# Kernel optimization log

Hardware: AMD Instinct MI355X
Metric: run time of the kernel (lower is better)

Reference implementation:

```python
import jax, jax.numpy as jnp
import numpy as np

H = 1024
NH = 16
HD = H // NH
EPS = 1e-5


def setup_inputs() -> dict:
    key = jax.random.key(0)
    ks = jax.random.split(key, 16)
    B, LQ, LK = 2, 1024, 2048
    s = 1.0 / np.sqrt(H)
    inp = {
        "query": jax.random.normal(ks[0], (B, LQ, H), jnp.float32),
        "key": jax.random.normal(ks[1], (B, LK, H), jnp.float32),
        "value": jax.random.normal(ks[2], (B, LK, H), jnp.float32),
        "mask": jax.random.randint(ks[3], (B, LQ, LK), 0, 2, jnp.int32),
        "Wq": jax.random.normal(ks[4], (H, H), jnp.float32) * s,
        "bq": jnp.zeros((H,), jnp.float32),
        "Wk": jax.random.normal(ks[5], (H, H), jnp.float32) * s,
        "bk": jnp.zeros((H,), jnp.float32),
        "Wv": jax.random.normal(ks[6], (H, H), jnp.float32) * s,
        "bv": jnp.zeros((H,), jnp.float32),
        "Wo": jax.random.normal(ks[7], (H, H), jnp.float32) * s,
        "bo": jnp.zeros((H,), jnp.float32),
        "ln_g": jnp.ones((H,), jnp.float32),
        "ln_b": jnp.zeros((H,), jnp.float32),
    }
    return inp


def _split_heads(x, B, L):
    # [B, L, H] -> [B, NH, L, HD]
    return x.reshape(B, L, NH, HD).transpose(0, 2, 1, 3)


def reference(query, key, value, mask, Wq, bq, Wk, bk, Wv, bv, Wo, bo, ln_g, ln_b):
    B, LQ, _ = query.shape
    LK = key.shape[1]
    # projections (torch Linear: x @ W.T + b)
    Q = _split_heads(query @ Wq.T + bq, B, LQ)   # [B,NH,LQ,HD]
    K = _split_heads(key   @ Wk.T + bk, B, LK)   # [B,NH,LK,HD]
    V = _split_heads(value @ Wv.T + bv, B, LK)   # [B,NH,LK,HD]
    scores = jnp.einsum('bhqd,bhkd->bhqk', Q, K) / np.sqrt(HD)
    scores = jnp.where(mask[:, None, :, :] == 0, jnp.float32(-1e9), scores)
    attn = jax.nn.softmax(scores, axis=-1)
    # dropout is identity in eval mode
    ctx = jnp.einsum('bhqk,bhkd->bhqd', attn, V)            # [B,NH,LQ,HD]
    ctx = ctx.transpose(0, 2, 1, 3).reshape(B, LQ, H)       # [B,LQ,H]
    out = ctx @ Wo.T + bo
    x = out + query
    mu = jnp.mean(x, axis=-1, keepdims=True)
    var = jnp.mean(jnp.square(x - mu), axis=-1, keepdims=True)
    return (x - mu) / jnp.sqrt(var + EPS) * ln_g + ln_b
```

## Files before the change

### kernel.cpp

```cpp
#include <hip/hip_runtime.h>
#include <hip/hip_bf16.h>

typedef __hip_bfloat16 hbf16;

#define Hdim 1024
#define NHEAD 16
#define HDIM 64
#define BATCH 2
#define LQ 1024
#define LK 2048
#define LN_EPS 1e-5f

typedef __bf16 bfv8 __attribute__((ext_vector_type(8)));
typedef float floatx4 __attribute__((ext_vector_type(4)));
typedef union { bfv8 v; __bf16 b[8]; unsigned short s[8]; } bfu8;

#define BK 32
#define LDS_PITCH 40
#define QT 64
#define KT 64
#define KS_PITCH 72
#define VT_OFF(d) ((d) * 72 + (((d) >> 3) << 3))
#define PS_OFF(r) ((r) * 72 + (((r) >> 2) << 3))

__device__ inline bfv8 cvt2(const float4 x, const float4 y) {
    bfv8 r = {(__bf16)x.x, (__bf16)x.y, (__bf16)x.z, (__bf16)x.w,
              (__bf16)y.x, (__bf16)y.y, (__bf16)y.z, (__bf16)y.w};
    return r;
}

__device__ __forceinline__ void glds16(const void* g, void* l) {
    __builtin_amdgcn_global_load_lds(
        (const __attribute__((address_space(1))) void*)g,
        (__attribute__((address_space(3))) void*)l, 16, 0, 0);
}

__global__ __launch_bounds__(256) void cvt_all(
    const float* __restrict__ q, const float* __restrict__ k,
    const float* __restrict__ v, const float* __restrict__ Wq,
    const float* __restrict__ Wk, const float* __restrict__ Wv,
    const int* __restrict__ mask,
    hbf16* __restrict__ qb, hbf16* __restrict__ kb, hbf16* __restrict__ vb,
    hbf16* __restrict__ Wqb, hbf16* __restrict__ Wkb, hbf16* __restrict__ Wvb,
    unsigned short* __restrict__ mpack) {
    const int blk = blockIdx.x;
    if (blk >= 6656) {
        const int t = blk - 6656;
        const int kt = t & 31;
        const int qb2 = (t >> 5) & 15;
        const int b2 = t >> 9;
        const int tid = threadIdx.x;
        const int w = tid >> 6;
        const int lane = tid & 63;
        const int quad = lane >> 4;
        const int u = lane & 15;
        const int qrow = qb2 * 64 + w * 16 + quad * 4;
        const int kcol = kt * 64 + u;
        const int* mp = mask + (size_t)(b2 * LQ + qrow) * LK + kcol;
        unsigned int bits = 0;
#pragma unroll
        for (int ns = 0; ns < 4; ++ns)
#pragma unroll
            for (int rr = 0; rr < 4; ++rr)
                if (mp[(size_t)rr * LK + ns * 16] != 0)
                    bits |= 1u << (ns * 4 + rr);
        mpack[(size_t)t * 256 + tid] = (unsigned short)bits;
        return;
    }
    const float* src; hbf16* dst; int base;
    if (blk < 1024)      { src = q;  dst = qb;  base = blk; }
    else if (blk < 3072) { src = k;  dst = kb;  base = blk - 1024; }
    else if (blk < 5120) { src = v;  dst = vb;  base = blk - 3072; }
    else if (blk < 5632) { src = Wq; dst = Wqb; base = blk - 5120; }
    else if (blk < 6144) { src = Wk; dst = Wkb; base = blk - 5632; }
    else                 { src = Wv; dst = Wvb; base = blk - 6144; }
    const size_t e = (size_t)base * 2048 + (size_t)threadIdx.x * 8;
    const float4 a = *(const float4*)(src + e);
    const float4 b = *(const float4*)(src + e + 4);
    *(bfv8*)((__bf16*)dst + e) = cvt2(a, b);
}

__global__ __launch_bounds__(256) void proj3_glds(
    const hbf16* __restrict__ qb, const hbf16* __restrict__ kb,
    const hbf16* __restrict__ vb,
    const hbf16* __restrict__ Wqb, const hbf16* __restrict__ Wkb,
    const hbf16* __restrict__ Wvb,
    const float* __restrict__ bq, const float* __restrict__ bk,
    const float* __restrict__ bv,
    hbf16* __restrict__ Qp, hbf16* __restrict__ Kp, hbf16* __restrict__ Vp) {
    const int z = blockIdx.z;
    if (z == 0 && blockIdx.y >= (BATCH * LQ) / 128) return;
    const hbf16* A; const hbf16* W; const float* bias; hbf16* out; float scale;
    if (z == 0)      { A = qb; W = Wqb; bias = bq; out = Qp; scale = 0.125f; }
    else if (z == 1) { A = kb; W = Wkb; bias = bk; out = Kp; scale = 1.0f; }
    else             { A = vb; W = Wvb; bias = bv; out = Vp; scale = 1.0f; }

    __shared__ __align__(16) __bf16 As[2][128 * 32];
    __shared__ __align__(16) __bf16 Bs[2][128 * 32];
    const int tid = threadIdx.x;
    const int lane = tid & 63;
    const int w = tid >> 6;
    const int wm = w & 1, wn = w >> 1;
    const int u = lane & 15;
    const int quad = lane >> 4;
    const int rowBase = blockIdx.y * 128;
    const int colBase = blockIdx.x * 128;

    const int srow = tid >> 2;
    const int scol = (tid & 3) * 8;
    const hbf16* aP = A + (size_t)(rowBase + srow) * Hdim + scol;
    const hbf16* wP = W + (size_t)(colBase + srow) * Hdim + scol;
    const int ldsOff = srow * 32 + scol;

#define P_STAGE(buf, k0)                                            \
    do {                                                            \
        glds16(aP + (k0), &As[buf][ldsOff]);                        \
        glds16(aP + (k0) + (size_t)64 * Hdim, &As[buf][ldsOff + 64 * 32]); \
        glds16(wP + (k0), &Bs[buf][ldsOff]);                        \
        glds16(wP + (k0) + (size_t)64 * Hdim, &Bs[buf][ldsOff + 64 * 32]); \
    } while (0)

    floatx4 acc[4][4];
#pragma unroll
    for (int mi = 0; mi < 4; ++mi)
#pragma unroll
        for (int ni = 0; ni < 4; ++ni) acc[mi][ni] = (floatx4){0.f, 0.f, 0.f, 0.f};

#define P_COMPUTE(buf)                                                         \
    do {                                                                       \
        bfv8 af[4], bf[4];                                                     \
        _Pragma("unroll") for (int mi = 0; mi < 4; ++mi)                       \
            af[mi] = *(const bfv8*)&As[buf][(wm * 64 + mi * 16 + u) * 32 + quad * 8]; \
        _Pragma("unroll") for (int ni = 0; ni < 4; ++ni)                       \
            bf[ni] = *(const bfv8*)&Bs[buf][(wn * 64 + ni * 16 + u) * 32 + quad * 8]; \
        _Pragma("unroll") for (int mi = 0; mi < 4; ++mi)                       \
            _Pragma("unroll") for (int ni = 0; ni < 4; ++ni)                   \
                acc[mi][ni] = __builtin_amdgcn_mfma_f32_16x16x32_bf16(af[mi], bf[ni], acc[mi][ni], 0, 0, 0); \
    } while (0)

    P_STAGE(0, 0);
    __syncthreads();

    for (int t = 0; t < 32; t += 2) {
        if (t + 1 < 32) P_STAGE(1, (t + 1) * 32);
        P_COMPUTE(0);
        __syncthreads();
        if (t + 2 < 32) P_STAGE(0, (t + 2) * 32);
        P_COMPUTE(1);
        __syncthreads();
    }
#undef P_STAGE
#undef P_COMPUTE

#pragma unroll
    for (int mi = 0; mi < 4; ++mi)
#pragma unroll
        for (int ni = 0; ni < 4; ++ni) {
            const int n = colBase + wn * 64 + ni * 16 + u;
            const float bn = bias[n];
#pragma unroll
            for (int rr = 0; rr < 4; ++rr) {
                const int m = rowBase + wm * 64 + mi * 16 + quad * 4 + rr;
                out[(size_t)m * Hdim + n] = __float2bfloat16((acc[mi][ni][rr] + bn) * scale);
            }
        }
}

__global__ __launch_bounds__(256) void gemm_ctx_merge(
    const float* __restrict__ Opart, const float* __restrict__ lpart,
    const float* __restrict__ W, const float* __restrict__ bias,
    const float* __restrict__ resid, float* __restrict__ out) {
    __shared__ __align__(16) __bf16 As[2][64 * 32];
    __shared__ __align__(16) __bf16 Bs[2][64 * 32];
    const int tid = threadIdx.x;
    const int lane = tid & 63;
    const int w = tid >> 6;
    const int wm = w & 1, wn = w >> 1;
    const int u = lane & 15;
    const int quad = lane >> 4;
    const int rowBase = blockIdx.y * 64;
    const int colBase = blockIdx.x * 64;

    const int srow = tid >> 2;
    const int scol = (tid & 3) * 8;
    const size_t mrow = (size_t)(rowBase + srow);
    const float* o0 = Opart + mrow * Hdim + scol;
    const float* o1 = o0 + (size_t)BATCH * LQ * Hdim;
    const float* lp0 = lpart + mrow * NHEAD;
    const float* lp1 = lp0 + BATCH * LQ * NHEAD;
    const float* wP = W + (size_t)(colBase + srow) * Hdim + scol;
    const int ldsOff = srow * 32 + scol;

    floatx4 acc[2][2];
#pragma unroll
    for (int mi = 0; mi < 2; ++mi)
#pragma unroll
        for (int ni = 0; ni < 2; ++ni) acc[mi][ni] = (floatx4){0.f, 0.f, 0.f, 0.f};

#define C_COMPUTE(buf)                                                         \
    do {                                                                       \
        bfv8 af[2], bf[2];                                                     \
        _Pragma("unroll") for (int mi = 0; mi < 2; ++mi)                       \
            af[mi] = *(const bfv8*)&As[buf][(wm * 32 + mi * 16 + u) * 32 + quad * 8]; \
        _Pragma("unroll") for (int ni = 0; ni < 2; ++ni)                       \
            bf[ni] = *(const bfv8*)&Bs[buf][(wn * 32 + ni * 16 + u) * 32 + quad * 8]; \
        _Pragma("unroll") for (int mi = 0; mi < 2; ++mi)                       \
            _Pragma("unroll") for (int ni = 0; ni < 2; ++ni)                   \
                acc[mi][ni] = __builtin_amdgcn_mfma_f32_16x16x32_bf16(af[mi], bf[ni], acc[mi][ni], 0, 0, 0); \
    } while (0)

#define M_WRITEA(buf, a0, a1, c0, c1, l0v, l1v)                                \
    do {                                                                       \
        const float invl_ = 1.0f / ((l0v) + (l1v));                            \
        float4 s0_, s1_;                                                       \
        s0_.x = (a0.x + c0.x) * invl_; s0_.y = (a0.y + c0.y) * invl_;          \
        s0_.z = (a0.z + c0.z) * invl_; s0_.w = (a0.w + c0.w) * invl_;          \
        s1_.x = (a1.x + c1.x) * invl_; s1_.y = (a1.y + c1.y) * invl_;          \
        s1_.z = (a1.z + c1.z) * invl_; s1_.w = (a1.w + c1.w) * invl_;          \
        *(bfv8*)&As[buf][ldsOff] = cvt2(s0_, s1_);                             \
    } while (0)

    {
        const float4 a0 = *(const float4*)(o0);
        const float4 a1 = *(const float4*)(o0 + 4);
        const float4 c0 = *(const float4*)(o1);
        const float4 c1 = *(const float4*)(o1 + 4);
        const int hh = scol >> 6;
        const float l0v = lp0[hh], l1v = lp1[hh];
        const float4* w4 = (const float4*)wP;
        const float4 w0 = w4[0], w1 = w4[1];
        M_WRITEA(0, a0, a1, c0, c1, l0v, l1v);
        *(bfv8*)&Bs[0][ldsOff] = cvt2(w0, w1);
    }
    __syncthreads();

    for (int t = 0; t < 32; t += 2) {
        {
            float4 a0, a1, c0, c1, w0, w1; float l0v = 1.f, l1v = 0.f;
            const bool pf = (t + 1 < 32);
            if (pf) {
                const int kk = (t + 1) * 32;
                a0 = *(const float4*)(o0 + kk);
                a1 = *(const float4*)(o0 + kk + 4);
                c0 = *(const float4*)(o1 + kk);
                c1 = *(const float4*)(o1 + kk + 4);
                const int hh = (kk + scol) >> 6;
                l0v = lp0[hh]; l1v = lp1[hh];
                const float4* w4 = (const float4*)(wP + kk);
                w0 = w4[0]; w1 = w4[1];
            }
            C_COMPUTE(0);
            if (pf) {
                M_WRITEA(1, a0, a1, c0, c1, l0v, l1v);
                *(bfv8*)&Bs[1][ldsOff] = cvt2(w0, w1);
            }
            __syncthreads();
        }
        {
            float4 a0, a1, c0, c1, w0, w1; float l0v = 1.f, l1v = 0.f;
            const bool pf = (t + 2 < 32);
            if (pf) {
                const int kk = (t + 2) * 32;
                a0 = *(const float4*)(o0 + kk);
                a1 = *(const float4*)(o0 + kk + 4);
                c0 = *(const float4*)(o1 + kk);
                c1 = *(const float4*)(o1 + kk + 4);
                const int hh = (kk + scol) >> 6;
                l0v = lp0[hh]; l1v = lp1[hh];
                const float4* w4 = (const float4*)(wP + kk);
                w0 = w4[0]; w1 = w4[1];
            }
            C_COMPUTE(1);
            if (pf) {
                M_WRITEA(0, a0, a1, c0, c1, l0v, l1v);
                *(bfv8*)&Bs[0][ldsOff] = cvt2(w0, w1);
            }
            __syncthreads();
        }
    }
#undef C_COMPUTE
#undef M_WRITEA

#pragma unroll
    for (int mi = 0; mi < 2; ++mi)
#pragma unroll
        for (int ni = 0; ni < 2; ++ni) {
            const int n = colBase + wn * 32 + ni * 16 + u;
            const float bn = bias[n];
#pragma unroll
            for (int rr = 0; rr < 4; ++rr) {
                const int m = rowBase + wm * 32 + mi * 16 + quad * 4 + rr;
                out[(size_t)m * Hdim + n] = acc[mi][ni][rr] + bn + resid[(size_t)m * Hdim + n];
            }
        }
}

__global__ __launch_bounds__(256) void proj3_mfma(
    const float* __restrict__ q_in, const float* __restrict__ k_in,
    const float* __restrict__ v_in,
    const float* __restrict__ Wq, const float* __restrict__ bq,
    const float* __restrict__ Wk, const float* __restrict__ bk,
    const float* __restrict__ Wv, const float* __restrict__ bv,
    hbf16* __restrict__ Qp, hbf16* __restrict__ Kp, hbf16* __restrict__ Vp) {
    const int z = blockIdx.z;
    if (z == 0 && blockIdx.y >= (BATCH * LQ) / 64) return;
    const float* A; const float* W; const float* bias; hbf16* out; float scale;
    if (z == 0)      { A = q_in; W = Wq; bias = bq; out = Qp; scale = 0.125f; }
    else if (z == 1) { A = k_in; W = Wk; bias = bk; out = Kp; scale = 1.0f; }
    else             { A = v_in; W = Wv; bias = bv; out = Vp; scale = 1.0f; }

    __shared__ __align__(16) __bf16 As[64 * LDS_PITCH];
    __shared__ __align__(16) __bf16 Bs[64 * LDS_PITCH];
    const int tid = threadIdx.x;
    const int lane = tid & 63;
    const int w = tid >> 6;
    const int wm = w & 1, wn = w >> 1;
    const int rowBase = blockIdx.y * 64;
    const int colBase = blockIdx.x * 64;
    const int sr = tid >> 2;
    const int scg = (tid & 3) * 8;
    const int lr = lane & 15;
    const int quad = lane >> 4;

    floatx4 acc[2][2] = {};

    for (int k0 = 0; k0 < Hdim; k0 += BK) {
        const float* ap = A + (size_t)(rowBase + sr) * Hdim + k0 + scg;
        bfv8 av = cvt2(((const float4*)ap)[0], ((const float4*)ap)[1]);
        const float* wp = W + (size_t)(colBase + sr) * Hdim + k0 + scg;
        bfv8 bv8 = cvt2(((const float4*)wp)[0], ((const float4*)wp)[1]);
        __syncthreads();
        *(bfv8*)&As[sr * LDS_PITCH + scg] = av;
        *(bfv8*)&Bs[sr * LDS_PITCH + scg] = bv8;
        __syncthreads();

        bfv8 bf[2];
#pragma unroll
        for (int nt = 0; nt < 2; ++nt)
            bf[nt] = *(const bfv8*)&Bs[(wn * 32 + nt * 16 + lr) * LDS_PITCH + quad * 8];
#pragma unroll
        for (int mt = 0; mt < 2; ++mt) {
            bfv8 af = *(const bfv8*)&As[(wm * 32 + mt * 16 + lr) * LDS_PITCH + quad * 8];
#pragma unroll
            for (int nt = 0; nt < 2; ++nt)
                acc[mt][nt] = __builtin_amdgcn_mfma_f32_16x16x32_bf16(af, bf[nt], acc[mt][nt], 0, 0, 0);
        }
    }

#pragma unroll
    for (int mt = 0; mt < 2; ++mt)
#pragma unroll
        for (int nt = 0; nt < 2; ++nt) {
            const int n = colBase + wn * 32 + nt * 16 + lr;
            const float bn = bias[n];
#pragma unroll
            for (int rr = 0; rr < 4; ++rr) {
                const int m = rowBase + wm * 32 + mt * 16 + quad * 4 + rr;
                out[(size_t)m * Hdim + n] = __float2bfloat16((acc[mt][nt][rr] + bn) * scale);
            }
        }
}

__global__ __launch_bounds__(256) void gemm_mfma_f32(const float* __restrict__ A,
                                                     const float* __restrict__ W,
                                                     const float* __restrict__ bias,
                                                     hbf16* __restrict__ out,
                                                     float scale) {
    __shared__ __align__(16) __bf16 As[64 * LDS_PITCH];
    __shared__ __align__(16) __bf16 Bs[64 * LDS_PITCH];
    const int tid = threadIdx.x;
    const int lane = tid & 63;
    const int w = tid >> 6;
    const int wm = w & 1, wn = w >> 1;
    const int rowBase = blockIdx.y * 64;
    const int colBase = blockIdx.x * 64;
    const int sr = tid >> 2;
    const int scg = (tid & 3) * 8;
    const int lr = lane & 15;
    const int quad = lane >> 4;

    floatx4 acc[2][2] = {};

    for (int k0 = 0; k0 < Hdim; k0 += BK) {
        const float* ap = A + (size_t)(rowBase + sr) * Hdim + k0 + scg;
        bfv8 av = cvt2(((const float4*)ap)[0], ((const float4*)ap)[1]);
        const float* wp = W + (size_t)(colBase + sr) * Hdim + k0 + scg;
        bfv8 bv = cvt2(((const float4*)wp)[0], ((const float4*)wp)[1]);
        __syncthreads();
        *(bfv8*)&As[sr * LDS_PITCH + scg] = av;
        *(bfv8*)&Bs[sr * LDS_PITCH + scg] = bv;
        __syncthreads();

        bfv8 bf[2];
#pragma unroll
        for (int nt = 0; nt < 2; ++nt)
            bf[nt] = *(const bfv8*)&Bs[(wn * 32 + nt * 16 + lr) * LDS_PITCH + quad * 8];
#pragma unroll
        for (int mt = 0; mt < 2; ++mt) {
            bfv8 af = *(const bfv8*)&As[(wm * 32 + mt * 16 + lr) * LDS_PITCH + quad * 8];
#pragma unroll
            for (int nt = 0; nt < 2; ++nt)
                acc[mt][nt] = __builtin_amdgcn_mfma_f32_16x16x32_bf16(af, bf[nt], acc[mt][nt], 0, 0, 0);
        }
    }

#pragma unroll
    for (int mt = 0; mt < 2; ++mt)
#pragma unroll
        for (int nt = 0; nt < 2; ++nt) {
            const int n = colBase + wn * 32 + nt * 16 + lr;
            const float bn = bias[n];
#pragma unroll
            for (int rr = 0; rr < 4; ++rr) {
                const int m = rowBase + wm * 32 + mt * 16 + quad * 4 + rr;
                out[(size_t)m * Hdim + n] = __float2bfloat16((acc[mt][nt][rr] + bn) * scale);
            }
        }
}

__global__ __launch_bounds__(256) void gemm_mfma_ctx(const hbf16* __restrict__ A,
                                                     const float* __restrict__ W,
                                                     const float* __restrict__ bias,
                                                     const float* __restrict__ resid,
                                                     float* __restrict__ out) {
    __shared__ __align__(16) __bf16 As[64 * LDS_PITCH];
    __shared__ __align__(16) __bf16 Bs[64 * LDS_PITCH];
    const int tid = threadIdx.x;
    const int lane = tid & 63;
    const int w = tid >> 6;
    const int wm = w & 1, wn = w >> 1;
    const int rowBase = blockIdx.y * 64;
    const int colBase = blockIdx.x * 64;
    const int sr = tid >> 2;
    const int scg = (tid & 3) * 8;
    const int lr = lane & 15;
    const int quad = lane >> 4;

    floatx4 acc[2][2] = {};

    for (int k0 = 0; k0 < Hdim; k0 += BK) {
        bfv8 av = *(const bfv8*)(A + (size_t)(rowBase + sr) * Hdim + k0 + scg);
        const float* wp = W + (size_t)(colBase + sr) * Hdim + k0 + scg;
        bfv8 bv = cvt2(((const float4*)wp)[0], ((const float4*)wp)[1]);
        __syncthreads();
        *(bfv8*)&As[sr * LDS_PITCH + scg] = av;
        *(bfv8*)&Bs[sr * LDS_PITCH + scg] = bv;
        __syncthreads();

        bfv8 bf[2];
#pragma unroll
        for (int nt = 0; nt < 2; ++nt)
            bf[nt] = *(const bfv8*)&Bs[(wn * 32 + nt * 16 + lr) * LDS_PITCH + quad * 8];
#pragma unroll
        for (int mt = 0; mt < 2; ++mt) {
            bfv8 af = *(const bfv8*)&As[(wm * 32 + mt * 16 + lr) * LDS_PITCH + quad * 8];
#pragma unroll
            for (int nt = 0; nt < 2; ++nt)
                acc[mt][nt] = __builtin_amdgcn_mfma_f32_16x16x32_bf16(af, bf[nt], acc[mt][nt], 0, 0, 0);
        }
    }

#pragma unroll
    for (int mt = 0; mt < 2; ++mt)
#pragma unroll
        for (int nt = 0; nt < 2; ++nt) {
            const int n = colBase + wn * 32 + nt * 16 + lr;
            const float bn = bias[n];
#pragma unroll
            for (int rr = 0; rr < 4; ++rr) {
                const int m = rowBase + wm * 32 + mt * 16 + quad * 4 + rr;
                out[(size_t)m * Hdim + n] = acc[mt][nt][rr] + bn + resid[(size_t)m * Hdim + n];
            }
        }
}

__global__ __launch_bounds__(256) void mask_prep_st(const int* __restrict__ mask,
                                                    hbf16* __restrict__ mbias) {
    const int t = blockIdx.x;
    const int kt = t & 31;
    const int qb = (t >> 5) & 15;
    const int b = t >> 9;
    const int tid = threadIdx.x;
    const int w = tid >> 6;
    const int lane = tid & 63;
    const int quad = lane >> 4;
    const int u = lane & 15;
    const int qrow = qb * 64 + w * 16 + quad * 4;
    const int kcol = kt * 64 + u;
    const int* mp = mask + ((size_t)(b * LQ + qrow)) * LK + kcol;

    bfu8 v0, v1;
#pragma unroll
    for (int ns = 0; ns < 4; ++ns)
#pragma unroll
        for (int rr = 0; rr < 4; ++rr) {
            const int mv = mp[(size_t)rr * LK + ns * 16];
            const __bf16 bias = (mv == 0) ? (__bf16)(-1e9f) : (__bf16)(-10.0f);
            const int j = ns * 4 + rr;
            if (j < 8) v0.b[j] = bias; else v1.b[j - 8] = bias;
        }
    __bf16* dst = (__bf16*)mbias + (size_t)t * 4096 + tid * 16;
    *(bfv8*)dst = v0.v;
    *(bfv8*)(dst + 8) = v1.v;
}

__global__ __launch_bounds__(256, 4) void attn_split(const hbf16* __restrict__ Qp,
                                                     const hbf16* __restrict__ Kp,
                                                     const hbf16* __restrict__ Vp,
                                                     const unsigned short* __restrict__ mpack,
                                                     float* __restrict__ Opart,
                                                     float* __restrict__ lpart) {
    const int wg = (blockIdx.x & 7) * 128 + (blockIdx.x >> 3);
    const int qb = wg & 15;
    const int h = (wg >> 4) & 15;
    const int z = wg >> 8;
    const int b = z >> 1;
    const int sp = z & 1;
    const int tid = threadIdx.x;
    const int lane = tid & 63;
    const int w = tid >> 6;
    const int u = lane & 15;
    const int quad = lane >> 4;
    const int qBase = qb * QT;

    __shared__ __align__(16) __bf16 Ks[64 * KS_PITCH];
    __shared__ __align__(16) __bf16 Vt[4672];
    __shared__ __align__(16) __bf16 Ps[4][1184];

    const int qrow_frag = qBase + w * 16 + u;
    const hbf16* qptr = Qp + (size_t)(b * LQ + qrow_frag) * Hdim + h * HDIM + quad * 8;
    const bfv8 af_q0 = *(const bfv8*)qptr;
    const bfv8 af_q1 = *(const bfv8*)(qptr + 32);

    float l_acc[4] = {0.f, 0.f, 0.f, 0.f};
    floatx4 acc_o[4];
#pragma unroll
    for (int nd = 0; nd < 4; ++nd) acc_o[nd] = (floatx4){0.f, 0.f, 0.f, 0.f};

    const int sk = tid >> 2;
    const int sdg = (tid & 3) * 16;
    const int vk2 = (tid >> 3) * 2;
    const int vd0 = (tid & 7) * 8;
    const unsigned short* mpk = mpack + (size_t)((b * 16 + qb) * 32) * 256 + tid;

    const int kt0 = sp * (LK / KT / 2);
    const int ktEnd = kt0 + (LK / KT / 2);

    unsigned int pmw;
    bfu8 pv0, pv1;
    bfv8 pk0, pk1;

#define A_LOADS(kt)                                                            \
    do {                                                                       \
        const int kBase_ = (kt) * KT;                                          \
        pmw = mpk[(size_t)(kt) * 256];                                         \
        const hbf16* vp_ = Vp + (size_t)(b * LK + kBase_ + vk2) * Hdim + h * HDIM + vd0; \
        pv0.v = *(const bfv8*)vp_;                                             \
        pv1.v = *(const bfv8*)(vp_ + Hdim);                                    \
        const hbf16* kp_ = Kp + (size_t)(b * LK + kBase_ + sk) * Hdim + h * HDIM + sdg; \
        pk0 = *(const bfv8*)kp_;                                               \
        pk1 = *(const bfv8*)(kp_ + 8);                                         \
    } while (0)

    A_LOADS(kt0);

    for (int kt = kt0; kt < ktEnd; ++kt) {
        __syncthreads();
        *(bfv8*)&Ks[sk * KS_PITCH + sdg] = pk0;
        *(bfv8*)&Ks[sk * KS_PITCH + sdg + 8] = pk1;
#pragma unroll
        for (int i = 0; i < 8; ++i) {
            unsigned int pk = (unsigned int)pv0.s[i] | ((unsigned int)pv1.s[i] << 16);
            *(unsigned int*)&Vt[VT_OFF(vd0 + i) + vk2] = pk;
        }
        const unsigned int mw = pmw;
        __syncthreads();

        if (kt + 1 < ktEnd) A_LOADS(kt + 1);

        floatx4 acc_s[4];
        __builtin_amdgcn_s_setprio(1);
#pragma unroll
        for (int ns = 0; ns < 4; ++ns) {
            const bfv8 bk0 = *(const bfv8*)&Ks[(ns * 16 + u) * KS_PITCH + quad * 8];
            const bfv8 bk1 = *(const bfv8*)&Ks[(ns * 16 + u) * KS_PITCH + quad * 8 + 32];
            floatx4 a = (floatx4){0.f, 0.f, 0.f, 0.f};
            a = __builtin_amdgcn_mfma_f32_16x16x32_bf16(af_q0, bk0, a, 0, 0, 0);
            a = __builtin_amdgcn_mfma_f32_16x16x32_bf16(af_q1, bk1, a, 0, 0, 0);
            acc_s[ns] = a;
        }
        __builtin_amdgcn_s_setprio(0);

        __bf16* Pw = Ps[w];
#pragma unroll
        for (int ns = 0; ns < 4; ++ns)
#pragma unroll
            for (int rr = 0; rr < 4; ++rr) {
                const int j = ns * 4 + rr;
                const float bias = ((mw >> j) & 1u) ? -10.0f : -1e9f;
                const float p = __expf(acc_s[ns][rr] + bias);
                Pw[PS_OFF(quad * 4 + rr) + ns * 16 + u] = (__bf16)p;
                l_acc[rr] += p;
            }

        const bfv8 af_p0 = *(const bfv8*)&Pw[PS_OFF(u) + quad * 8];
        const bfv8 af_p1 = *(const bfv8*)&Pw[PS_OFF(u) + quad * 8 + 32];
        __builtin_amdgcn_s_setprio(1);
#pragma unroll
        for (int nd = 0; nd < 4; ++nd) {
            const bfv8 bv0 = *(const bfv8*)&Vt[VT_OFF(nd * 16 + u) + quad * 8];
            const bfv8 bv1 = *(const bfv8*)&Vt[VT_OFF(nd * 16 + u) + quad * 8 + 32];
            acc_o[nd] = __builtin_amdgcn_mfma_f32_16x16x32_bf16(af_p0, bv0, acc_o[nd], 0, 0, 0);
            acc_o[nd] = __builtin_amdgcn_mfma_f32_16x16x32_bf16(af_p1, bv1, acc_o[nd], 0, 0, 0);
        }
        __builtin_amdgcn_s_setprio(0);
    }
#undef A_LOADS

#pragma unroll
    for (int rr = 0; rr < 4; ++rr) {
        float l = l_acc[rr];
        l += __shfl_xor(l, 1, 64);
        l += __shfl_xor(l, 2, 64);
        l += __shfl_xor(l, 4, 64);
        l += __shfl_xor(l, 8, 64);
        const int qrow = qBase + w * 16 + quad * 4 + rr;
        const size_t m = (size_t)(b * LQ + qrow);
        float* orow = Opart + (size_t)sp * (BATCH * LQ * Hdim) + m * Hdim + h * HDIM;
#pragma unroll
        for (int nd = 0; nd < 4; ++nd)
            orow[nd * 16 + u] = acc_o[nd][rr];
        if (u == 0)
            lpart[(size_t)sp * (BATCH * LQ * NHEAD) + m * NHEAD + h] = l;
    }
}

__global__ __launch_bounds__(256, 4) void attn_flash_st(const hbf16* __restrict__ Qp,
                                                        const hbf16* __restrict__ Kp,
                                                        const hbf16* __restrict__ Vp,
                                                        const hbf16* __restrict__ mbias,
                                                        hbf16* __restrict__ ctx) {
    const int qb = blockIdx.x;
    const int h = blockIdx.y;
    const int b = blockIdx.z;
    const int tid = threadIdx.x;
    const int lane = tid & 63;
    const int w = tid >> 6;
    const int u = lane & 15;
    const int quad = lane >> 4;
    const int qBase = qb * QT;

    __shared__ __align__(16) __bf16 Ks[64 * KS_PITCH];
    __shared__ __align__(16) __bf16 Vt[4672];
    __shared__ __align__(16) __bf16 Ps[4][1184];

    const int qrow_frag = qBase + w * 16 + u;
    const hbf16* qptr = Qp + (size_t)(b * LQ + qrow_frag) * Hdim + h * HDIM + quad * 8;
    const bfv8 af_q0 = *(const bfv8*)qptr;
    const bfv8 af_q1 = *(const bfv8*)(qptr + 32);

    float l_acc[4] = {0.f, 0.f, 0.f, 0.f};
    floatx4 acc_o[4];
#pragma unroll
    for (int nd = 0; nd < 4; ++nd) acc_o[nd] = (floatx4){0.f, 0.f, 0.f, 0.f};

    const int sk = tid >> 2;
    const int sdg = (tid & 3) * 16;
    const int vk2 = (tid >> 3) * 2;
    const int vd0 = (tid & 7) * 8;
    const __bf16* mbT = (const __bf16*)mbias + (size_t)(b * 16 + qb) * 32 * 4096 + tid * 16;

    for (int kt = 0; kt < LK / KT; ++kt) {
        const int kBase = kt * KT;

        bfu8 mb0, mb1;
        mb0.v = *(const bfv8*)(mbT + (size_t)kt * 4096);
        mb1.v = *(const bfv8*)(mbT + (size_t)kt * 4096 + 8);

        const hbf16* vp0 = Vp + (size_t)(b * LK + kBase + vk2) * Hdim + h * HDIM + vd0;
        bfu8 v0, v1;
        v0.v = *(const bfv8*)vp0;
        v1.v = *(const bfv8*)(vp0 + Hdim);
        const hbf16* kp = Kp + (size_t)(b * LK + kBase + sk) * Hdim + h * HDIM + sdg;
        const bfv8 kv0 = *(const bfv8*)kp;
        const bfv8 kv1 = *(const bfv8*)(kp + 8);

        __syncthreads();
        *(bfv8*)&Ks[sk * KS_PITCH + sdg] = kv0;
        *(bfv8*)&Ks[sk * KS_PITCH + sdg + 8] = kv1;
#pragma unroll
        for (int i = 0; i < 8; ++i) {
            unsigned int pk = (unsigned int)v0.s[i] | ((unsigned int)v1.s[i] << 16);
            *(unsigned int*)&Vt[VT_OFF(vd0 + i) + vk2] = pk;
        }
        __syncthreads();

        floatx4 acc_s[4];
#pragma unroll
        for (int ns = 0; ns < 4; ++ns) {
            const bfv8 bk0 = *(const bfv8*)&Ks[(ns * 16 + u) * KS_PITCH + quad * 8];
            const bfv8 bk1 = *(const bfv8*)&Ks[(ns * 16 + u) * KS_PITCH + quad * 8 + 32];
            floatx4 a = (floatx4){0.f, 0.f, 0.f, 0.f};
            a = __builtin_amdgcn_mfma_f32_16x16x32_bf16(af_q0, bk0, a, 0, 0, 0);
            a = __builtin_amdgcn_mfma_f32_16x16x32_bf16(af_q1, bk1, a, 0, 0, 0);
            acc_s[ns] = a;
        }

        __bf16* Pw = Ps[w];
#pragma unroll
        for (int ns = 0; ns < 4; ++ns)
#pragma unroll
            for (int rr = 0; rr < 4; ++rr) {
                const int j = ns * 4 + rr;
                const float bias = (j < 8) ? (float)mb0.b[j] : (float)mb1.b[j - 8];
                const float p = __expf(acc_s[ns][rr] + bias);
                Pw[PS_OFF(quad * 4 + rr) + ns * 16 + u] = (__bf16)p;
                l_acc[rr] += p;
            }

        const bfv8 af_p0 = *(const bfv8*)&Pw[PS_OFF(u) + quad * 8];
        const bfv8 af_p1 = *(const bfv8*)&Pw[PS_OFF(u) + quad * 8 + 32];
#pragma unroll
        for (int nd = 0; nd < 4; ++nd) {
            const bfv8 bv0 = *(const bfv8*)&Vt[VT_OFF(nd * 16 + u) + quad * 8];
            const bfv8 bv1 = *(const bfv8*)&Vt[VT_OFF(nd * 16 + u) + quad * 8 + 32];
            acc_o[nd] = __builtin_amdgcn_mfma_f32_16x16x32_bf16(af_p0, bv0, acc_o[nd], 0, 0, 0);
            acc_o[nd] = __builtin_amdgcn_mfma_f32_16x16x32_bf16(af_p1, bv1, acc_o[nd], 0, 0, 0);
        }
    }

#pragma unroll
    for (int rr = 0; rr < 4; ++rr) {
        float l = l_acc[rr];
        l += __shfl_xor(l, 1, 64);
        l += __shfl_xor(l, 2, 64);
        l += __shfl_xor(l, 4, 64);
        l += __shfl_xor(l, 8, 64);
        const float invl = 1.0f / l;
        const int qrow = qBase + w * 16 + quad * 4 + rr;
        hbf16* crow = ctx + (size_t)(b * LQ + qrow) * Hdim + h * HDIM;
#pragma unroll
        for (int nd = 0; nd < 4; ++nd)
            crow[nd * 16 + u] = __float2bfloat16(acc_o[nd][rr] * invl);
    }
}

__global__ __launch_bounds__(256) void ln_kernel(float* __restrict__ x,
                                                 const float* __restrict__ g,
                                                 const float* __restrict__ beta) {
    const int row = blockIdx.x;
    float* xr = x + (size_t)row * Hdim;
    __shared__ float red[256];
    const int tid = threadIdx.x;

    const float4 xi = ((const float4*)xr)[tid];
    red[tid] = xi.x + xi.y + xi.z + xi.w;
    __syncthreads();
    for (int st = 128; st > 0; st >>= 1) {
        if (tid < st) red[tid] += red[tid + st];
        __syncthreads();
    }
    const float mu = red[0] * (1.0f / Hdim);
    __syncthreads();
    {
        float dx = xi.x - mu, dy = xi.y - mu, dz = xi.z - mu, dw = xi.w - mu;
        red[tid] = dx * dx + dy * dy + dz * dz + dw * dw;
    }
    __syncthreads();
    for (int st = 128; st > 0; st >>= 1) {
        if (tid < st) red[tid] += red[tid + st];
        __syncthreads();
    }
    const float rstd = rsqrtf(red[0] * (1.0f / Hdim) + LN_EPS);

    const float4 g4 = ((const float4*)g)[tid];
    const float4 b4 = ((const float4*)beta)[tid];
    float4 y;
    y.x = (xi.x - mu) * rstd * g4.x + b4.x;
    y.y = (xi.y - mu) * rstd * g4.y + b4.y;
    y.z = (xi.z - mu) * rstd * g4.z + b4.z;
    y.w = (xi.w - mu) * rstd * g4.w + b4.w;
    ((float4*)xr)[tid] = y;
}

__device__ inline float wave_red_sum(float v) {
    v += __shfl_down(v, 32, 64);
    v += __shfl_down(v, 16, 64);
    v += __shfl_down(v, 8, 64);
    v += __shfl_down(v, 4, 64);
    v += __shfl_down(v, 2, 64);
    v += __shfl_down(v, 1, 64);
    return v;
}

__global__ __launch_bounds__(256) void fused_mha(
    const float* __restrict__ q_in, const float* __restrict__ k_in,
    const float* __restrict__ v_in, const int* __restrict__ mask,
    const float* __restrict__ Wq, const float* __restrict__ bq,
    const float* __restrict__ Wk, const float* __restrict__ bk,
    const float* __restrict__ Wv, const float* __restrict__ bv,
    const float* __restrict__ Wo, const float* __restrict__ bo,
    const float* __restrict__ ln_g, const float* __restrict__ ln_b,
    float* __restrict__ out) {
    const int q = blockIdx.x;
    const int b = blockIdx.y;
    const int tid = threadIdx.x;
    const int lane = tid & 63;
    const int w = tid >> 6;

    __shared__ float qrow[Hdim];
    __shared__ float qt[Hdim];
    __shared__ float sc[LK];
    __shared__ float u[Hdim];
    __shared__ float ctxv[Hdim];
    __shared__ float Qh[HDIM];
    __shared__ float red[256];
    __shared__ float sb_sh;

    const float* qp = q_in + (size_t)(b * LQ + q) * Hdim;
    for (int i = tid; i < Hdim; i += 256) qrow[i] = qp[i];
    __syncthreads();

    const float* keyb = k_in + (size_t)b * LK * Hdim;
    const float* valb = v_in + (size_t)b * LK * Hdim;
    const int* mrow = mask + (size_t)(b * LQ + q) * LK;

    for (int h = 0; h < NHEAD; ++h) {
        for (int dd = w; dd < HDIM; dd += 4) {
            const float4* wrow = (const float4*)(Wq + (size_t)(h * HDIM + dd) * Hdim);
            const float4* q4 = (const float4*)qrow;
            float p = 0.f;
#pragma unroll
            for (int i0 = 0; i0 < 4; ++i0) {
                float4 a = wrow[i0 * 64 + lane];
                float4 c = q4[i0 * 64 + lane];
                p += a.x * c.x + a.y * c.y + a.z * c.z + a.w * c.w;
            }
            p = wave_red_sum(p);
            if (lane == 0) Qh[dd] = p + bq[h * HDIM + dd];
        }
        __syncthreads();

        if (tid < HDIM) red[tid] = Qh[tid] * bk[h * HDIM + tid];

        float4 s4 = {0.f, 0.f, 0.f, 0.f};
        for (int d = 0; d < HDIM; ++d) {
            float4 a = ((const float4*)(Wk + (size_t)(h * HDIM + d) * Hdim))[tid];
            float qd = Qh[d];
            s4.x += a.x * qd;
            s4.y += a.y * qd;
            s4.z += a.z * qd;
            s4.w += a.w * qd;
        }
        __syncthreads();
        if (tid == 0) {
            float s = 0.f;
            for (int i = 0; i < HDIM; ++i) s += red[i];
            sb_sh = s;
        }
        ((float4*)qt)[tid] = s4;
        __syncthreads();
        const float sb = sb_sh;

        for (int k = w; k < LK; k += 4) {
            const float4* krow = (const float4*)(keyb + (size_t)k * Hdim);
            const float4* q4 = (const float4*)qt;
            float p = 0.f;
#pragma unroll
            for (int i0 = 0; i0 < 4; ++i0) {
                float4 a = krow[i0 * 64 + lane];
                float4 c = q4[i0 * 64 + lane];
                p += a.x * c.x + a.y * c.y + a.z * c.z + a.w * c.w;
            }
            p = wave_red_sum(p);
            if (lane == 0) {
                float s = (p + sb) * 0.125f;
                if (mrow[k] == 0) s = -1e9f;
                sc[k] = s;
            }
        }
        __syncthreads();

        float m = -1e30f;
        for (int k = tid; k < LK; k += 256) m = fmaxf(m, sc[k]);
        red[tid] = m;
        __syncthreads();
        for (int s = 128; s > 0; s >>= 1) {
            if (tid < s) red[tid] = fmaxf(red[tid], red[tid + s]);
            __syncthreads();
        }
        const float mx = red[0];
        __syncthreads();
        float sum = 0.f;
        for (int k = tid; k < LK; k += 256) {
            float e = __expf(sc[k] - mx);
            sc[k] = e;
            sum += e;
        }
        red[tid] = sum;
        __syncthreads();
        for (int s = 128; s > 0; s >>= 1) {
            if (tid < s) red[tid] += red[tid + s];
            __syncthreads();
        }
        const float inv = 1.0f / red[0];
        for (int k = tid; k < LK; k += 256) sc[k] *= inv;
        __syncthreads();

        {
            float4 acc = {0.f, 0.f, 0.f, 0.f};
            const float4* vb4 = (const float4*)valb;
#pragma unroll 4
            for (int k = 0; k < LK; ++k) {
                float p = sc[k];
                float4 a = vb4[(size_t)k * (Hdim / 4) + tid];
                acc.x += a.x * p;
                acc.y += a.y * p;
                acc.z += a.z * p;
                acc.w += a.w * p;
            }
            ((float4*)u)[tid] = acc;
        }
        __syncthreads();

        for (int dd = w; dd < HDIM; dd += 4) {
            const float4* wrow = (const float4*)(Wv + (size_t)(h * HDIM + dd) * Hdim);
            const float4* u4 = (const float4*)u;
            float p = 0.f;
#pragma unroll
            for (int i0 = 0; i0 < 4; ++i0) {
                float4 a = wrow[i0 * 64 + lane];
                float4 c = u4[i0 * 64 + lane];
                p += a.x * c.x + a.y * c.y + a.z * c.z + a.w * c.w;
            }
            p = wave_red_sum(p);
            if (lane == 0) ctxv[h * HDIM + dd] = p + bv[h * HDIM + dd];
        }
        __syncthreads();
    }

    for (int n = w; n < Hdim; n += 4) {
        const float4* wrow = (const float4*)(Wo + (size_t)n * Hdim);
        const float4* c4 = (const float4*)ctxv;
        float p = 0.f;
#pragma unroll
        for (int i0 = 0; i0 < 4; ++i0) {
            float4 a = wrow[i0 * 64 + lane];
            float4 c = c4[i0 * 64 + lane];
            p += a.x * c.x + a.y * c.y + a.z * c.z + a.w * c.w;
        }
        p = wave_red_sum(p);
        if (lane == 0) qt[n] = p + bo[n] + qrow[n];
    }
    __syncthreads();

    {
        const float4 x4 = ((const float4*)qt)[tid];
        red[tid] = x4.x + x4.y + x4.z + x4.w;
    }
    __syncthreads();
    for (int s = 128; s > 0; s >>= 1) {
        if (tid < s) red[tid] += red[tid + s];
        __syncthreads();
    }
    const float mu = red[0] * (1.0f / Hdim);
    __syncthreads();
    {
        const float4 x4 = ((const float4*)qt)[tid];
        float dx = x4.x - mu, dy = x4.y - mu, dz = x4.z - mu, dw = x4.w - mu;
        red[tid] = dx * dx + dy * dy + dz * dz + dw * dw;
    }
    __syncthreads();
    for (int s = 128; s > 0; s >>= 1) {
        if (tid < s) red[tid] += red[tid + s];
        __syncthreads();
    }
    const float rstd = rsqrtf(red[0] * (1.0f / Hdim) + LN_EPS);

    float* orow = out + (size_t)(b * LQ + q) * Hdim;
    const float4 x4 = ((const float4*)qt)[tid];
    const float4 g4 = ((const float4*)ln_g)[tid];
    const float4 b4 = ((const float4*)ln_b)[tid];
    float4 y;
    y.x = (x4.x - mu) * rstd * g4.x + b4.x;
    y.y = (x4.y - mu) * rstd * g4.y + b4.y;
    y.z = (x4.z - mu) * rstd * g4.z + b4.z;
    y.w = (x4.w - mu) * rstd * g4.w + b4.w;
    ((float4*)orow)[tid] = y;
}

extern "C" void kernel_launch(void* const* d_in, const int* in_sizes, int n_in,
                              void* d_out, int out_size, void* d_ws, size_t ws_size,
                              hipStream_t stream) {
    const float* query = (const float*)d_in[0];
    const float* key   = (const float*)d_in[1];
    const float* value = (const float*)d_in[2];
    const int*   mask  = (const int*)d_in[3];
    const float* Wq = (const float*)d_in[4];
    const float* bq = (const float*)d_in[5];
    const float* Wk = (const float*)d_in[6];
    const float* bk = (const float*)d_in[7];
    const float* Wv = (const float*)d_in[8];
    const float* bv = (const float*)d_in[9];
    const float* Wo = (const float*)d_in[10];
    const float* bo = (const float*)d_in[11];
    const float* ln_g = (const float*)d_in[12];
    const float* ln_b = (const float*)d_in[13];
    float* out = (float*)d_out;

    const size_t MB = 1024 * 1024;
    dim3 blk(256);

    if (ws_size >= 50 * MB) {
        char* p = (char*)d_ws;
        hbf16* Qp    = (hbf16*)(p + 0 * MB);
        hbf16* Kp    = (hbf16*)(p + 4 * MB);
        hbf16* Vp    = (hbf16*)(p + 12 * MB);
        float* Opart = (float*)(p + 20 * MB);
        unsigned short* mpack = (unsigned short*)(p + 46 * MB);
        float* lpart = (float*)(p + 47 * MB);

        hbf16* qb  = (hbf16*)(p + 20 * MB);
        hbf16* kb  = (hbf16*)(p + 24 * MB);
        hbf16* vb  = (hbf16*)(p + 32 * MB);
        hbf16* Wqb = (hbf16*)(p + 40 * MB);
        hbf16* Wkb = (hbf16*)(p + 42 * MB);
        hbf16* Wvb = (hbf16*)(p + 44 * MB);

        cvt_all<<<dim3(7680), blk, 0, stream>>>(query, key, value, Wq, Wk, Wv,
                                                mask, qb, kb, vb, Wqb, Wkb, Wvb,
                                                mpack);
        proj3_glds<<<dim3(Hdim / 128, (BATCH * LK) / 128, 3), blk, 0, stream>>>(
            qb, kb, vb, Wqb, Wkb, Wvb, bq, bk, bv, Qp, Kp, Vp);

        attn_split<<<dim3(1024), blk, 0, stream>>>(
            Qp, Kp, Vp, mpack, Opart, lpart);

        gemm_ctx_merge<<<dim3(Hdim / 64, (BATCH * LQ) / 64), blk, 0, stream>>>(
            Opart, lpart, Wo, bo, query, out);
        ln_kernel<<<BATCH * LQ, blk, 0, stream>>>(out, ln_g, ln_b);
    } else if (ws_size >= 32 * MB) {
        char* p = (char*)d_ws;
        hbf16* Qp = (hbf16*)p;    p += 4 * MB;
        hbf16* Kp = (hbf16*)p;    p += 8 * MB;
        hbf16* Vp = (hbf16*)p;    p += 8 * MB;
        hbf16* ctxb = (hbf16*)p;  p += 4 * MB;
        hbf16* mbias = (hbf16*)p; p += 8 * MB;

        gemm_mfma_f32<<<dim3(Hdim / 64, (BATCH * LQ) / 64), blk, 0, stream>>>(query, Wq, bq, Qp, 0.125f);
        gemm_mfma_f32<<<dim3(Hdim / 64, (BATCH * LK) / 64), blk, 0, stream>>>(key, Wk, bk, Kp, 1.0f);
        gemm_mfma_f32<<<dim3(Hdim / 64, (BATCH * LK) / 64), blk, 0, stream>>>(value, Wv, bv, Vp, 1.0f);
        mask_prep_st<<<dim3(1024), blk, 0, stream>>>(mask, mbias);
        attn_flash_st<<<dim3(LQ / QT, NHEAD, BATCH), blk, 0, stream>>>(Qp, Kp, Vp, mbias, ctxb);
        gemm_mfma_ctx<<<dim3(Hdim / 64, (BATCH * LQ) / 64), blk, 0, stream>>>(ctxb, Wo, bo, query, out);
        ln_kernel<<<BATCH * LQ, blk, 0, stream>>>(out, ln_g, ln_b);
    } else {
        fused_mha<<<dim3(LQ, BATCH), dim3(256), 0, stream>>>(
            query, key, value, mask, Wq, bq, Wk, bk, Wv, bv, Wo, bo, ln_g, ln_b, out);
    }
}
```

Measured before the change: 240.8 us.

## Fuse fp32-to-bf16 activation conversion into projection GEMM A-tile loads

The separate conversion pass over query/key/value is removed. The projection kernel now loads fp32 activations directly, converts them in registers and writes bf16 into LDS, overlapping this with the MFMA compute on the other buffer. The prep kernel now only converts the weights and packs the mask. The projection grid is also flattened into 640 blocks with a swizzled block-to-tile mapping and no idle Q blocks. This saves a full write and read of the bf16 activation copies, but the A-tile loads go through registers instead of direct global-to-LDS, which adds register pressure and VALU work inside the GEMM loop.

```diff
diff --git a/kernel.cpp b/kernel.cpp
--- a/kernel.cpp
+++ b/kernel.cpp
@@ -35,65 +35,62 @@
         (__attribute__((address_space(3))) void*)l, 16, 0, 0);
 }
 
-__global__ __launch_bounds__(256) void cvt_all(
-    const float* __restrict__ q, const float* __restrict__ k,
-    const float* __restrict__ v, const float* __restrict__ Wq,
-    const float* __restrict__ Wk, const float* __restrict__ Wv,
-    const int* __restrict__ mask,
-    hbf16* __restrict__ qb, hbf16* __restrict__ kb, hbf16* __restrict__ vb,
+__global__ __launch_bounds__(256) void prep_wmask(
+    const float* __restrict__ Wq, const float* __restrict__ Wk,
+    const float* __restrict__ Wv, const int* __restrict__ mask,
     hbf16* __restrict__ Wqb, hbf16* __restrict__ Wkb, hbf16* __restrict__ Wvb,
     unsigned short* __restrict__ mpack) {
     const int blk = blockIdx.x;
-    if (blk >= 6656) {
-        const int t = blk - 6656;
-        const int kt = t & 31;
-        const int qb2 = (t >> 5) & 15;
-        const int b2 = t >> 9;
-        const int tid = threadIdx.x;
-        const int w = tid >> 6;
-        const int lane = tid & 63;
-        const int quad = lane >> 4;
-        const int u = lane & 15;
-        const int qrow = qb2 * 64 + w * 16 + quad * 4;
-        const int kcol = kt * 64 + u;
-        const int* mp = mask + (size_t)(b2 * LQ + qrow) * LK + kcol;
-        unsigned int bits = 0;
-#pragma unroll
-        for (int ns = 0; ns < 4; ++ns)
-#pragma unroll
-            for (int rr = 0; rr < 4; ++rr)
-                if (mp[(size_t)rr * LK + ns * 16] != 0)
-                    bits |= 1u << (ns * 4 + rr);
-        mpack[(size_t)t * 256 + tid] = (unsigned short)bits;
+    if (blk < 1536) {
+        const float* src; hbf16* dst; int base;
+        if (blk < 512)       { src = Wq; dst = Wqb; base = blk; }
+        else if (blk < 1024) { src = Wk; dst = Wkb; base = blk - 512; }
+        else                 { src = Wv; dst = Wvb; base = blk - 1024; }
+        const size_t e = (size_t)base * 2048 + (size_t)threadIdx.x * 8;
+        const float4 a = *(const float4*)(src + e);
+        const float4 b = *(const float4*)(src + e + 4);
+        *(bfv8*)((__bf16*)dst + e) = cvt2(a, b);
         return;
     }
-    const float* src; hbf16* dst; int base;
-    if (blk < 1024)      { src = q;  dst = qb;  base = blk; }
-    else if (blk < 3072) { src = k;  dst = kb;  base = blk - 1024; }
-    else if (blk < 5120) { src = v;  dst = vb;  base = blk - 3072; }
-    else if (blk < 5632) { src = Wq; dst = Wqb; base = blk - 5120; }
-    else if (blk < 6144) { src = Wk; dst = Wkb; base = blk - 5632; }
-    else                 { src = Wv; dst = Wvb; base = blk - 6144; }
-    const size_t e = (size_t)base * 2048 + (size_t)threadIdx.x * 8;
-    const float4 a = *(const float4*)(src + e);
-    const float4 b = *(const float4*)(src + e + 4);
-    *(bfv8*)((__bf16*)dst + e) = cvt2(a, b);
-}
-
-__global__ __launch_bounds__(256) void proj3_glds(
-    const hbf16* __restrict__ qb, const hbf16* __restrict__ kb,
-    const hbf16* __restrict__ vb,
+    const int t = blk - 1536;
+    const int kt = t & 31;
+    const int qb2 = (t >> 5) & 15;
+    const int b2 = t >> 9;
+    const int tid = threadIdx.x;
+    const int w = tid >> 6;
+    const int lane = tid & 63;
+    const int quad = lane >> 4;
+    const int u = lane & 15;
+    const int qrow = qb2 * 64 + w * 16 + quad * 4;
+    const int kcol = kt * 64 + u;
+    const int* mp = mask + (size_t)(b2 * LQ + qrow) * LK + kcol;
+    unsigned int bits = 0;
+#pragma unroll
+    for (int ns = 0; ns < 4; ++ns)
+#pragma unroll
+        for (int rr = 0; rr < 4; ++rr)
+            if (mp[(size_t)rr * LK + ns * 16] != 0)
+                bits |= 1u << (ns * 4 + rr);
+    mpack[(size_t)t * 256 + tid] = (unsigned short)bits;
+}
+
+__global__ __launch_bounds__(256) void proj3_f32(
+    const float* __restrict__ q_in, const float* __restrict__ k_in,
+    const float* __restrict__ v_in,
     const hbf16* __restrict__ Wqb, const hbf16* __restrict__ Wkb,
     const hbf16* __restrict__ Wvb,
     const float* __restrict__ bq, const float* __restrict__ bk,
     const float* __restrict__ bv,
     hbf16* __restrict__ Qp, hbf16* __restrict__ Kp, hbf16* __restrict__ Vp) {
-    const int z = blockIdx.z;
-    if (z == 0 && blockIdx.y >= (BATCH * LQ) / 128) return;
-    const hbf16* A; const hbf16* W; const float* bias; hbf16* out; float scale;
-    if (z == 0)      { A = qb; W = Wqb; bias = bq; out = Qp; scale = 0.125f; }
-    else if (z == 1) { A = kb; W = Wkb; bias = bk; out = Kp; scale = 1.0f; }
-    else             { A = vb; W = Wvb; bias = bv; out = Vp; scale = 1.0f; }
+    const int wg = (blockIdx.x & 7) * 80 + (blockIdx.x >> 3);
+    int z, x, y;
+    if (wg < 128)      { z = 0; x = wg & 7; y = wg >> 3; }
+    else if (wg < 384) { z = 1; x = (wg - 128) & 7; y = (wg - 128) >> 3; }
+    else               { z = 2; x = (wg - 384) & 7; y = (wg - 384) >> 3; }
+    const float* A; const hbf16* W; const float* bias; hbf16* out; float scale;
+    if (z == 0)      { A = q_in; W = Wqb; bias = bq; out = Qp; scale = 0.125f; }
+    else if (z == 1) { A = k_in; W = Wkb; bias = bk; out = Kp; scale = 1.0f; }
+    else             { A = v_in; W = Wvb; bias = bv; out = Vp; scale = 1.0f; }
 
     __shared__ __align__(16) __bf16 As[2][128 * 32];
     __shared__ __align__(16) __bf16 Bs[2][128 * 32];
@@ -103,21 +100,23 @@
     const int wm = w & 1, wn = w >> 1;
     const int u = lane & 15;
     const int quad = lane >> 4;
-    const int rowBase = blockIdx.y * 128;
-    const int colBase = blockIdx.x * 128;
+    const int rowBase = y * 128;
+    const int colBase = x * 128;
+
+    const int arow = tid >> 1;
+    const int acol = (tid & 1) * 16;
+    const float* aPf = A + (size_t)(rowBase + arow) * Hdim + acol;
+    const int ldsOffA = arow * 32 + acol;
 
     const int srow = tid >> 2;
     const int scol = (tid & 3) * 8;
-    const hbf16* aP = A + (size_t)(rowBase + srow) * Hdim + scol;
     const hbf16* wP = W + (size_t)(colBase + srow) * Hdim + scol;
-    const int ldsOff = srow * 32 + scol;
-
-#define P_STAGE(buf, k0)                                            \
-    do {                                                            \
-        glds16(aP + (k0), &As[buf][ldsOff]);                        \
-        glds16(aP + (k0) + (size_t)64 * Hdim, &As[buf][ldsOff + 64 * 32]); \
-        glds16(wP + (k0), &Bs[buf][ldsOff]);                        \
-        glds16(wP + (k0) + (size_t)64 * Hdim, &Bs[buf][ldsOff + 64 * 32]); \
+    const int ldsOffB = srow * 32 + scol;
+
+#define PB_STAGE(buf, k0)                                                \
+    do {                                                                 \
+        glds16(wP + (k0), &Bs[buf][ldsOffB]);                            \
+        glds16(wP + (k0) + (size_t)64 * Hdim, &Bs[buf][ldsOffB + 64 * 32]); \
     } while (0)
 
     floatx4 acc[4][4];
@@ -138,18 +137,48 @@
                 acc[mi][ni] = __builtin_amdgcn_mfma_f32_16x16x32_bf16(af[mi], bf[ni], acc[mi][ni], 0, 0, 0); \
     } while (0)
 
-    P_STAGE(0, 0);
+    {
+        const float4* a4 = (const float4*)aPf;
+        const float4 a0 = a4[0], a1 = a4[1], a2 = a4[2], a3 = a4[3];
+        PB_STAGE(0, 0);
+        *(bfv8*)&As[0][ldsOffA] = cvt2(a0, a1);
+        *(bfv8*)&As[0][ldsOffA + 8] = cvt2(a2, a3);
+    }
     __syncthreads();
 
     for (int t = 0; t < 32; t += 2) {
-        if (t + 1 < 32) P_STAGE(1, (t + 1) * 32);
-        P_COMPUTE(0);
-        __syncthreads();
-        if (t + 2 < 32) P_STAGE(0, (t + 2) * 32);
-        P_COMPUTE(1);
-        __syncthreads();
-    }
-#undef P_STAGE
+        {
+            float4 a0, a1, a2, a3;
+            const bool pf = (t + 1 < 32);
+            if (pf) {
+                const float4* a4 = (const float4*)(aPf + (t + 1) * 32);
+                a0 = a4[0]; a1 = a4[1]; a2 = a4[2]; a3 = a4[3];
+                PB_STAGE(1, (t + 1) * 32);
+            }
+            P_COMPUTE(0);
+            if (pf) {
+                *(bfv8*)&As[1][ldsOffA] = cvt2(a0, a1);
+                *(bfv8*)&As[1][ldsOffA + 8] = cvt2(a2, a3);
+            }
+            __syncthreads();
+        }
+        {
+            float4 a0, a1, a2, a3;
+            const bool pf = (t + 2 < 32);
+            if (pf) {
+                const float4* a4 = (const float4*)(aPf + (t + 2) * 32);
+                a0 = a4[0]; a1 = a4[1]; a2 = a4[2]; a3 = a4[3];
+                PB_STAGE(0, (t + 2) * 32);
+            }
+            P_COMPUTE(1);
+            if (pf) {
+                *(bfv8*)&As[0][ldsOffA] = cvt2(a0, a1);
+                *(bfv8*)&As[0][ldsOffA + 8] = cvt2(a2, a3);
+            }
+            __syncthreads();
+        }
+    }
+#undef PB_STAGE
 #undef P_COMPUTE
 
 #pragma unroll
@@ -1017,21 +1046,16 @@
         hbf16* Kp    = (hbf16*)(p + 4 * MB);
         hbf16* Vp    = (hbf16*)(p + 12 * MB);
         float* Opart = (float*)(p + 20 * MB);
+        hbf16* Wqb   = (hbf16*)(p + 40 * MB);
+        hbf16* Wkb   = (hbf16*)(p + 42 * MB);
+        hbf16* Wvb   = (hbf16*)(p + 44 * MB);
         unsigned short* mpack = (unsigned short*)(p + 46 * MB);
         float* lpart = (float*)(p + 47 * MB);
 
-        hbf16* qb  = (hbf16*)(p + 20 * MB);
-        hbf16* kb  = (hbf16*)(p + 24 * MB);
-        hbf16* vb  = (hbf16*)(p + 32 * MB);
-        hbf16* Wqb = (hbf16*)(p + 40 * MB);
-        hbf16* Wkb = (hbf16*)(p + 42 * MB);
-        hbf16* Wvb = (hbf16*)(p + 44 * MB);
-
-        cvt_all<<<dim3(7680), blk, 0, stream>>>(query, key, value, Wq, Wk, Wv,
-                                                mask, qb, kb, vb, Wqb, Wkb, Wvb,
-                                                mpack);
-        proj3_glds<<<dim3(Hdim / 128, (BATCH * LK) / 128, 3), blk, 0, stream>>>(
-            qb, kb, vb, Wqb, Wkb, Wvb, bq, bk, bv, Qp, Kp, Vp);
+        prep_wmask<<<dim3(2560), blk, 0, stream>>>(Wq, Wk, Wv, mask,
+                                                   Wqb, Wkb, Wvb, mpack);
+        proj3_f32<<<dim3(640), blk, 0, stream>>>(
+            query, key, value, Wqb, Wkb, Wvb, bq, bk, bv, Qp, Kp, Vp);
 
         attn_split<<<dim3(1024), blk, 0, stream>>>(
             Qp, Kp, Vp, mpack, Opart, lpart);
```

After: 269.6 us. 1.12x slower.
